# Optimization experiments

Measured on AMD Instinct MI355X. Metric: run time of the kernel, lower is better.

Reference implementation:

```python
import jax, jax.numpy as jnp
import numpy as np

DECAY = 0.99


def setup_inputs() -> dict:
    key = jax.random.key(0)
    k1, k2, k3 = jax.random.split(key, 3)
    B, L, D, N = 8, 2048, 512, 1024
    x = jax.random.normal(k1, (B, L, D), dtype=jnp.float32)
    codebook = jax.random.normal(k2, (N, D), dtype=jnp.float32)
    ema_weight = jax.random.normal(k3, (N, D), dtype=jnp.float32)
    counts = jnp.ones((N,), dtype=jnp.float32)
    return {"x": x, "codebook": codebook, "ema_weight": ema_weight, "counts": counts}


def reference(x, codebook, ema_weight, counts):
    # x: [B, L, D]; codebook/ema_weight: [N, D]; counts: [N]
    n_tokens = codebook.shape[0]
    # avoids materializing the [B,L,N,D] difference tensor of the naive form)
    x_sq = jnp.sum(x * x, axis=-1, keepdims=True)            # [B, L, 1]
    c_sq = jnp.sum(codebook * codebook, axis=-1)             # [N]
    xc = jnp.einsum('bld,nd->bln', x, codebook)              # [B, L, N]
    distances = jnp.sqrt(jnp.maximum(x_sq - 2.0 * xc + c_sq, 0.0))
    indices = jnp.argmin(distances, axis=-1)                 # [B, L]
    encodings = jax.nn.one_hot(indices, n_tokens, dtype=jnp.float32)  # [B, L, N]
    # train=True branch: EMA codebook update
    counts_new = DECAY * counts + (1.0 - DECAY) * jnp.sum(encodings, axis=(0, 1))
    dw = jnp.einsum('bln,bld->nd', encodings, x)             # [N, D]
    ema_new = DECAY * ema_weight + (1.0 - DECAY) * dw
    codebook_new = ema_new / counts_new[:, None]
    # quantization with straight-through estimator
    quantized = jnp.einsum('bln,nd->bld', encodings, codebook_new)  # [B, L, D]
    quantized = x + jax.lax.stop_gradient(quantized - x)
    # optax.l2_loss(x, quantized) = 0.5 * (x - quantized)^2
    codebook_loss = jnp.mean(0.5 * jnp.square(x - quantized))
    return quantized, codebook_loss, indices
```

## Files before the change

kernel.cpp:

```cpp
#include <hip/hip_runtime.h>
#include <hip/hip_bf16.h>

constexpr int Dd   = 512;
constexpr int Nn   = 1024;
constexpr int Ttok = 16384;
constexpr float DECAYc = 0.99f;
constexpr float MARGIN = 10.0f;
constexpr int CH = 16;

typedef short bf16x8 __attribute__((ext_vector_type(8)));
typedef float f32x4  __attribute__((ext_vector_type(4)));
typedef unsigned short us8v __attribute__((ext_vector_type(8)));

__device__ inline unsigned short f2bf(float f) {
  unsigned int b = __float_as_uint(f);
  return (unsigned short)((b + 0x7FFFu + ((b >> 16) & 1u)) >> 16);
}
__device__ inline float bf2f(unsigned short u) {
  return __uint_as_float(((unsigned int)u) << 16);
}

__global__ __launch_bounds__(64) void k_prep_cb(const float* __restrict__ cb,
                                                unsigned short* __restrict__ cbh,
                                                float* __restrict__ csq) {
  const int n = blockIdx.x, l = threadIdx.x;
  const float4* r = (const float4*)(cb + (size_t)n * Dd);
  float4 a = r[l], b = r[l + 64];
  float ss = a.x*a.x + a.y*a.y + a.z*a.z + a.w*a.w
           + b.x*b.x + b.y*b.y + b.z*b.z + b.w*b.w;
  ushort4 ua, ub;
  ua.x = f2bf(a.x); ua.y = f2bf(a.y); ua.z = f2bf(a.z); ua.w = f2bf(a.w);
  ub.x = f2bf(b.x); ub.y = f2bf(b.y); ub.z = f2bf(b.z); ub.w = f2bf(b.w);
  ((ushort4*)(cbh + (size_t)n * Dd))[l]      = ua;
  ((ushort4*)(cbh + (size_t)n * Dd))[l + 64] = ub;
#pragma unroll
  for (int o = 32; o; o >>= 1) ss += __shfl_down(ss, o);
  if (l == 0) csq[n] = ss;
}

__global__ __launch_bounds__(256) void k_gemm_scores(
    const unsigned short* __restrict__ cbh, const float* __restrict__ x,
    const float* __restrict__ csq, unsigned short* __restrict__ S) {
  __shared__ unsigned short As[128 * 64];
  __shared__ unsigned short Bs[128 * 64];
  const int tid = threadIdx.x;
  const int w = tid >> 6, l = tid & 63;
  const int b = blockIdx.x;
  const int s = (b & 7) * 128 + (b >> 3);
  const int cm = s & 7;
  const int tn = s >> 3;
  const int wr = w >> 1, wc = w & 1;

  const int srow = tid >> 3;
  const int scol = (tid & 7) * 8;

  f32x4 acc[4][4] = {};

  const unsigned short* gA0 = cbh + (size_t)(cm * 128) * Dd;
  const float*          gB0 = x   + (size_t)(tn * 128) * Dd;

  for (int kc = 0; kc < Dd / 64; ++kc) {
    const int k0 = kc * 64;
    __syncthreads();
#pragma unroll
    for (int c = 0; c < 4; ++c) {
      const unsigned short* ga = gA0 + (size_t)(c * 32 + srow) * Dd + k0 + scol;
      char* la = (char*)As + c * 4096 + w * 1024;
      __builtin_amdgcn_global_load_lds((const __attribute__((address_space(1))) void*)ga,
                                       (__attribute__((address_space(3))) void*)la, 16, 0, 0);
    }
#pragma unroll
    for (int p = 0; p < 4; ++p) {
      const int r = p * 32 + srow;
      const float* gb = gB0 + (size_t)r * Dd + k0 + scol;
      float4 v0 = *(const float4*)gb;
      float4 v1 = *(const float4*)(gb + 4);
      us8v o;
      o[0] = f2bf(v0.x); o[1] = f2bf(v0.y); o[2] = f2bf(v0.z); o[3] = f2bf(v0.w);
      o[4] = f2bf(v1.x); o[5] = f2bf(v1.y); o[6] = f2bf(v1.z); o[7] = f2bf(v1.w);
      *(us8v*)&Bs[r * 64 + scol] = o;
    }
    __syncthreads();
#pragma unroll
    for (int ks = 0; ks < 2; ++ks) {
      const int kb = ks * 32 + (l >> 4) * 8;
      const int ra = l & 15;
      bf16x8 af[4], bfr[4];
#pragma unroll
      for (int m = 0; m < 4; ++m)
        af[m] = *(const bf16x8*)&As[(wr * 64 + m * 16 + ra) * 64 + kb];
#pragma unroll
      for (int n = 0; n < 4; ++n)
        bfr[n] = *(const bf16x8*)&Bs[(wc * 64 + n * 16 + ra) * 64 + kb];
#pragma unroll
      for (int m = 0; m < 4; ++m)
#pragma unroll
        for (int n = 0; n < 4; ++n)
          acc[m][n] = __builtin_amdgcn_mfma_f32_16x16x32_bf16(af[m], bfr[n], acc[m][n], 0, 0, 0);
    }
  }

  const int code0 = cm * 128 + wr * 64 + (l >> 4) * 4;
  const int tok0  = tn * 128 + wc * 64 + (l & 15);
#pragma unroll
  for (int m = 0; m < 4; ++m) {
    const int cd = code0 + m * 16;
    float4 cs = *(const float4*)&csq[cd];
#pragma unroll
    for (int n = 0; n < 4; ++n) {
      const int tk = tok0 + n * 16;
      ushort4 o;
      o.x = f2bf(cs.x - 2.0f * acc[m][n][0]);
      o.y = f2bf(cs.y - 2.0f * acc[m][n][1]);
      o.z = f2bf(cs.z - 2.0f * acc[m][n][2]);
      o.w = f2bf(cs.w - 2.0f * acc[m][n][3]);
      *(ushort4*)(S + (size_t)tk * Nn + cd) = o;
    }
  }
}

__global__ __launch_bounds__(256) void k_scan(
    const unsigned short* __restrict__ S, const float* __restrict__ x,
    const float* __restrict__ cb, const float* __restrict__ csq,
    int* __restrict__ idxb, float* __restrict__ idxf, float* __restrict__ hist) {
  __shared__ int candn[4][32];
  __shared__ int ccnt[4];
  const int tid = threadIdx.x, wid = tid >> 6, l = tid & 63;
  const int t = blockIdx.x * 4 + wid;

  const unsigned short* row = S + (size_t)t * Nn;
  us8v c0 = *(const us8v*)(row + l * 8);
  us8v c1 = *(const us8v*)(row + 512 + l * 8);
  float f0[8], f1[8];
  float minv = 3.4e38f; int mini = 0;
#pragma unroll
  for (int j = 0; j < 8; ++j) {
    f0[j] = bf2f(c0[j]);
    if (f0[j] < minv) { minv = f0[j]; mini = l * 8 + j; }
  }
#pragma unroll
  for (int j = 0; j < 8; ++j) {
    f1[j] = bf2f(c1[j]);
    if (f1[j] < minv) { minv = f1[j]; mini = 512 + l * 8 + j; }
  }
#pragma unroll
  for (int o = 1; o < 64; o <<= 1) {
    float ov = __shfl_xor(minv, o); int oi = __shfl_xor(mini, o);
    if (ov < minv || (ov == minv && oi < mini)) { minv = ov; mini = oi; }
  }
  if (l == 0) ccnt[wid] = 0;
  const float thr = minv + MARGIN;
#pragma unroll
  for (int j = 0; j < 8; ++j)
    if (f0[j] <= thr) { int p = atomicAdd(&ccnt[wid], 1); if (p < 32) candn[wid][p] = l * 8 + j; }
#pragma unroll
  for (int j = 0; j < 8; ++j)
    if (f1[j] <= thr) { int p = atomicAdd(&ccnt[wid], 1); if (p < 32) candn[wid][p] = 512 + l * 8 + j; }
  int nc = ccnt[wid]; if (nc > 32) nc = 32;

  int besti;
  if (nc == 1) {
    besti = candn[wid][0];
  } else {
    float bestv = 3.4e38f; besti = 0x7fffffff;
    const float4* xr = (const float4*)(x + (size_t)t * Dd);
    float4 xa = xr[l * 2], xb = xr[l * 2 + 1];
    for (int c = 0; c < nc; ++c) {
      int n = candn[wid][c];
      const float4* cr = (const float4*)(cb + (size_t)n * Dd);
      float4 ca = cr[l * 2], cb4 = cr[l * 2 + 1];
      float p = xa.x*ca.x + xa.y*ca.y + xa.z*ca.z + xa.w*ca.w
              + xb.x*cb4.x + xb.y*cb4.y + xb.z*cb4.z + xb.w*cb4.w;
#pragma unroll
      for (int o = 32; o; o >>= 1) p += __shfl_xor(p, o);
      float sc = csq[n] - 2.0f * p;
      if (sc < bestv || (sc == bestv && n < besti)) { bestv = sc; besti = n; }
    }
  }
  if (l == 0) {
    idxb[t] = besti;
    idxf[t] = (float)besti;
    atomicAdd(&hist[besti], 1.0f);
  }
}

__global__ __launch_bounds__(1024) void k_offsets(const float* __restrict__ hist,
                                                  int* __restrict__ offs,
                                                  int* __restrict__ cursor) {
  __shared__ int sh[1024];
  const int tid = threadIdx.x;
  const int c = (int)hist[tid];
  sh[tid] = c; __syncthreads();
  for (int o = 1; o < 1024; o <<= 1) {
    int a = (tid >= o) ? sh[tid - o] : 0;
    __syncthreads();
    sh[tid] += a;
    __syncthreads();
  }
  const int excl = sh[tid] - c;
  offs[tid] = excl; cursor[tid] = excl;
}

__global__ __launch_bounds__(256) void k_scatter(const int* __restrict__ idxb,
                                                 int* __restrict__ cursor,
                                                 int* __restrict__ bucket,
                                                 int* __restrict__ bcode) {
  int t = blockIdx.x * 256 + threadIdx.x;
  if (t < Ttok) {
    int n = idxb[t];
    int p = atomicAdd(&cursor[n], 1);
    bucket[p] = t;
    bcode[p] = n;
  }
}

__global__ __launch_bounds__(512) void k_dw_part(
    const float* __restrict__ x, const int* __restrict__ bucket,
    const int* __restrict__ bcode, float* __restrict__ dw) {
  __shared__ int sh_t[CH], sh_n[CH];
  const int tid = threadIdx.x;
  const int p0 = blockIdx.x * CH;
  if (tid < CH) { sh_t[tid] = bucket[p0 + tid]; sh_n[tid] = bcode[p0 + tid]; }
  __syncthreads();
  float v[CH];
#pragma unroll
  for (int j = 0; j < CH; ++j)
    v[j] = x[(size_t)sh_t[j] * Dd + tid];
  float acc = v[0]; int cur = sh_n[0];
#pragma unroll
  for (int j = 1; j < CH; ++j) {
    int n = sh_n[j];
    if (n != cur) { atomicAdd(&dw[(size_t)cur * Dd + tid], acc); acc = 0.f; cur = n; }
    acc += v[j];
  }
  atomicAdd(&dw[(size_t)cur * Dd + tid], acc);
}

__global__ __launch_bounds__(256) void finalize_cb(
    const float* __restrict__ ema, const float* __restrict__ dw,
    const float* __restrict__ counts, const float* __restrict__ hist,
    float* __restrict__ cbnew) {
  int e4 = blockIdx.x * 256 + threadIdx.x;
  int n = e4 >> 7;
  float cnt = DECAYc * counts[n] + (1.0f - DECAYc) * hist[n];
  float inv = 1.0f / cnt;
  float4 e = ((const float4*)ema)[e4];
  float4 d = ((const float4*)dw)[e4];
  float4 o;
  o.x = (DECAYc * e.x + (1.0f - DECAYc) * d.x) * inv;
  o.y = (DECAYc * e.y + (1.0f - DECAYc) * d.y) * inv;
  o.z = (DECAYc * e.z + (1.0f - DECAYc) * d.z) * inv;
  o.w = (DECAYc * e.w + (1.0f - DECAYc) * d.w) * inv;
  ((float4*)cbnew)[e4] = o;
}

__global__ __launch_bounds__(256) void quant_loss(
    const float* __restrict__ x, const float* __restrict__ cbnew,
    const int* __restrict__ idx, float* __restrict__ out_q,
    float* __restrict__ loss) {
  float part = 0.f;
  const int total4 = Ttok * Dd / 4;
  for (int e4 = blockIdx.x * 256 + threadIdx.x; e4 < total4;
       e4 += gridDim.x * 256) {
    int t = e4 >> 7, d4 = e4 & 127;
    int n = idx[t];
    float4 q = ((const float4*)(cbnew + (size_t)n * Dd))[d4];
    float4 xv = ((const float4*)x)[e4];
    ((float4*)out_q)[e4] = q;
    float dx = xv.x - q.x, dy = xv.y - q.y, dz = xv.z - q.z, dw_ = xv.w - q.w;
    part += dx*dx + dy*dy + dz*dz + dw_*dw_;
  }
  __shared__ float red[4];
#pragma unroll
  for (int o = 32; o; o >>= 1) part += __shfl_down(part, o);
  int wid = threadIdx.x >> 6, lane = threadIdx.x & 63;
  if (lane == 0) red[wid] = part;
  __syncthreads();
  if (threadIdx.x == 0) atomicAdd(loss, red[0] + red[1] + red[2] + red[3]);
}

__global__ void loss_final(const float* __restrict__ loss,
                           float* __restrict__ out_loss) {
  *out_loss = loss[0] * (0.5f / (float)((size_t)Ttok * Dd));
}

extern "C" void kernel_launch(void* const* d_in, const int* in_sizes, int n_in,
                              void* d_out, int out_size, void* d_ws, size_t ws_size,
                              hipStream_t stream) {
  const float* x      = (const float*)d_in[0];
  const float* cb     = (const float*)d_in[1];
  const float* ema    = (const float*)d_in[2];
  const float* counts = (const float*)d_in[3];

  float* out      = (float*)d_out;
  float* q_out    = out;
  float* loss_out = out + (size_t)Ttok * Dd;
  float* idxf_out = loss_out + 1;
  unsigned short* S = (unsigned short*)q_out;

  float* ws = (float*)d_ws;
  unsigned short* cbh = (unsigned short*)ws;
  float* dw     = ws + 262144;
  float* hist   = ws + 786432;
  float* loss   = ws + 787456;
  float* csq    = ws + 787460;
  int*   offs   = (int*)(ws + 788484);
  int*   cursor = (int*)(ws + 789508);
  int*   bucket = (int*)(ws + 790532);
  int*   bcode  = (int*)(ws + 806916);
  int*   idxb   = (int*)(ws + 823300);
  float* cbnew  = ws + 839684;

  hipMemsetAsync(dw, 0, (size_t)525316 * sizeof(float), stream);

  k_prep_cb<<<Nn, 64, 0, stream>>>(cb, cbh, csq);
  k_gemm_scores<<<(Nn / 128) * (Ttok / 128), 256, 0, stream>>>(cbh, x, csq, S);
  k_scan<<<Ttok / 4, 256, 0, stream>>>(S, x, cb, csq, idxb, idxf_out, hist);
  k_offsets<<<1, 1024, 0, stream>>>(hist, offs, cursor);
  k_scatter<<<Ttok / 256, 256, 0, stream>>>(idxb, cursor, bucket, bcode);
  k_dw_part<<<Ttok / CH, 512, 0, stream>>>(x, bucket, bcode, dw);
  finalize_cb<<<(Nn * Dd / 4) / 256, 256, 0, stream>>>(ema, dw, counts, hist, cbnew);
  quant_loss<<<2048, 256, 0, stream>>>(x, cbnew, idxb, q_out, loss);
  loss_final<<<1, 1, 0, stream>>>(loss, loss_out);
}
```

Baseline: 135.5 us.

## Swizzle GEMM LDS, prefetch x tile into registers, simplify scan, fuse loss finalize

The scores GEMM now XOR-swizzles the LDS column layout for both A and B tiles to avoid bank conflicts, and prefetches the next k-chunk of x (converted to bf16) into registers while the current chunk is multiplied. The offsets scan drops to 256 threads using wave shuffles in place of a barrier-heavy shared-memory scan. The separate loss_final launch is removed: the last block of quant_loss, found through an atomic counter, writes the normalized loss. Together these aim to cut LDS stalls, global-load latency and launch overhead, at the cost of more registers in the GEMM. The counter relies on the existing memset.

```diff
diff --git a/kernel.cpp b/kernel.cpp
--- a/kernel.cpp
+++ b/kernel.cpp
@@ -52,46 +52,60 @@
   const int wr = w >> 1, wc = w & 1;
 
   const int srow = tid >> 3;
-  const int scol = (tid & 7) * 8;
+  const int xorw = (tid >> 3) & 7;
+  const int scolA = ((tid & 7) ^ xorw) * 8;
+  const int scolB = (tid & 7) * 8;
+  const int wcolB = ((tid & 7) ^ xorw) * 8;
 
   f32x4 acc[4][4] = {};
 
   const unsigned short* gA0 = cbh + (size_t)(cm * 128) * Dd;
   const float*          gB0 = x   + (size_t)(tn * 128) * Dd;
+
+  us8v bq[4];
+#define LOADB(KC) do {                                                        \
+    const int k0_ = (KC) * 64;                                                \
+    _Pragma("unroll")                                                         \
+    for (int p = 0; p < 4; ++p) {                                             \
+      const float* gb = gB0 + (size_t)(p * 32 + srow) * Dd + k0_ + scolB;     \
+      float4 v0 = *(const float4*)gb;                                         \
+      float4 v1 = *(const float4*)(gb + 4);                                   \
+      us8v o;                                                                 \
+      o[0]=f2bf(v0.x); o[1]=f2bf(v0.y); o[2]=f2bf(v0.z); o[3]=f2bf(v0.w);     \
+      o[4]=f2bf(v1.x); o[5]=f2bf(v1.y); o[6]=f2bf(v1.z); o[7]=f2bf(v1.w);     \
+      bq[p] = o;                                                              \
+    }                                                                         \
+  } while (0)
+
+  LOADB(0);
 
   for (int kc = 0; kc < Dd / 64; ++kc) {
     const int k0 = kc * 64;
     __syncthreads();
 #pragma unroll
     for (int c = 0; c < 4; ++c) {
-      const unsigned short* ga = gA0 + (size_t)(c * 32 + srow) * Dd + k0 + scol;
+      const unsigned short* ga = gA0 + (size_t)(c * 32 + srow) * Dd + k0 + scolA;
       char* la = (char*)As + c * 4096 + w * 1024;
       __builtin_amdgcn_global_load_lds((const __attribute__((address_space(1))) void*)ga,
                                        (__attribute__((address_space(3))) void*)la, 16, 0, 0);
     }
 #pragma unroll
-    for (int p = 0; p < 4; ++p) {
-      const int r = p * 32 + srow;
-      const float* gb = gB0 + (size_t)r * Dd + k0 + scol;
-      float4 v0 = *(const float4*)gb;
-      float4 v1 = *(const float4*)(gb + 4);
-      us8v o;
-      o[0] = f2bf(v0.x); o[1] = f2bf(v0.y); o[2] = f2bf(v0.z); o[3] = f2bf(v0.w);
-      o[4] = f2bf(v1.x); o[5] = f2bf(v1.y); o[6] = f2bf(v1.z); o[7] = f2bf(v1.w);
-      *(us8v*)&Bs[r * 64 + scol] = o;
-    }
+    for (int p = 0; p < 4; ++p)
+      *(us8v*)&Bs[(p * 32 + srow) * 64 + wcolB] = bq[p];
     __syncthreads();
+    if (kc + 1 < Dd / 64) LOADB(kc + 1);
 #pragma unroll
     for (int ks = 0; ks < 2; ++ks) {
-      const int kb = ks * 32 + (l >> 4) * 8;
       const int ra = l & 15;
+      const int rx = l & 7;
+      const int kbs = ((ks * 4 + (l >> 4)) ^ rx) * 8;
       bf16x8 af[4], bfr[4];
 #pragma unroll
       for (int m = 0; m < 4; ++m)
-        af[m] = *(const bf16x8*)&As[(wr * 64 + m * 16 + ra) * 64 + kb];
+        af[m] = *(const bf16x8*)&As[(wr * 64 + m * 16 + ra) * 64 + kbs];
 #pragma unroll
       for (int n = 0; n < 4; ++n)
-        bfr[n] = *(const bf16x8*)&Bs[(wc * 64 + n * 16 + ra) * 64 + kb];
+        bfr[n] = *(const bf16x8*)&Bs[(wc * 64 + n * 16 + ra) * 64 + kbs];
 #pragma unroll
       for (int m = 0; m < 4; ++m)
 #pragma unroll
@@ -99,6 +113,7 @@
           acc[m][n] = __builtin_amdgcn_mfma_f32_16x16x32_bf16(af[m], bfr[n], acc[m][n], 0, 0, 0);
     }
   }
+#undef LOADB
 
   const int code0 = cm * 128 + wr * 64 + (l >> 4) * 4;
   const int tok0  = tn * 128 + wc * 64 + (l & 15);
@@ -184,21 +199,27 @@
   }
 }
 
-__global__ __launch_bounds__(1024) void k_offsets(const float* __restrict__ hist,
-                                                  int* __restrict__ offs,
-                                                  int* __restrict__ cursor) {
-  __shared__ int sh[1024];
-  const int tid = threadIdx.x;
-  const int c = (int)hist[tid];
-  sh[tid] = c; __syncthreads();
-  for (int o = 1; o < 1024; o <<= 1) {
-    int a = (tid >= o) ? sh[tid - o] : 0;
-    __syncthreads();
-    sh[tid] += a;
-    __syncthreads();
-  }
-  const int excl = sh[tid] - c;
-  offs[tid] = excl; cursor[tid] = excl;
+__global__ __launch_bounds__(256) void k_offsets(const float* __restrict__ hist,
+                                                 int* __restrict__ offs,
+                                                 int* __restrict__ cursor) {
+  __shared__ int wsum[4];
+  const int tid = threadIdx.x, l = tid & 63, wd = tid >> 6;
+  const int base = tid * 4;
+  int c0 = (int)hist[base], c1 = (int)hist[base + 1],
+      c2 = (int)hist[base + 2], c3 = (int)hist[base + 3];
+  int sum = c0 + c1 + c2 + c3;
+  int sc = sum;
+#pragma unroll
+  for (int o = 1; o < 64; o <<= 1) { int v = __shfl_up(sc, o); if (l >= o) sc += v; }
+  if (l == 63) wsum[wd] = sc;
+  __syncthreads();
+  int wbase = 0;
+  for (int i = 0; i < wd; ++i) wbase += wsum[i];
+  int e = wbase + sc - sum;
+  offs[base] = e;     cursor[base] = e;
+  offs[base+1] = e + c0; cursor[base+1] = e + c0;
+  offs[base+2] = e + c0 + c1; cursor[base+2] = e + c0 + c1;
+  offs[base+3] = e + c0 + c1 + c2; cursor[base+3] = e + c0 + c1 + c2;
 }
 
 __global__ __launch_bounds__(256) void k_scatter(const int* __restrict__ idxb,
@@ -257,7 +278,8 @@
 __global__ __launch_bounds__(256) void quant_loss(
     const float* __restrict__ x, const float* __restrict__ cbnew,
     const int* __restrict__ idx, float* __restrict__ out_q,
-    float* __restrict__ loss) {
+    float* __restrict__ loss, int* __restrict__ counter,
+    float* __restrict__ out_loss) {
   float part = 0.f;
   const int total4 = Ttok * Dd / 4;
   for (int e4 = blockIdx.x * 256 + threadIdx.x; e4 < total4;
@@ -276,12 +298,13 @@
   int wid = threadIdx.x >> 6, lane = threadIdx.x & 63;
   if (lane == 0) red[wid] = part;
   __syncthreads();
-  if (threadIdx.x == 0) atomicAdd(loss, red[0] + red[1] + red[2] + red[3]);
-}
-
-__global__ void loss_final(const float* __restrict__ loss,
-                           float* __restrict__ out_loss) {
-  *out_loss = loss[0] * (0.5f / (float)((size_t)Ttok * Dd));
+  if (threadIdx.x == 0) {
+    atomicAdd(loss, red[0] + red[1] + red[2] + red[3]);
+    __threadfence();
+    int prev = atomicAdd(counter, 1);
+    if (prev == (int)gridDim.x - 1)
+      *out_loss = *loss * (0.5f / (float)((size_t)Ttok * Dd));
+  }
 }
 
 extern "C" void kernel_launch(void* const* d_in, const int* in_sizes, int n_in,
@@ -300,26 +323,26 @@
 
   float* ws = (float*)d_ws;
   unsigned short* cbh = (unsigned short*)ws;
-  float* dw     = ws + 262144;
-  float* hist   = ws + 786432;
-  float* loss   = ws + 787456;
-  float* csq    = ws + 787460;
-  int*   offs   = (int*)(ws + 788484);
-  int*   cursor = (int*)(ws + 789508);
-  int*   bucket = (int*)(ws + 790532);
-  int*   bcode  = (int*)(ws + 806916);
-  int*   idxb   = (int*)(ws + 823300);
-  float* cbnew  = ws + 839684;
+  float* dw      = ws + 262144;
+  float* hist    = ws + 786432;
+  float* loss    = ws + 787456;
+  int*   counter = (int*)(ws + 787457);
+  float* csq     = ws + 787460;
+  int*   offs    = (int*)(ws + 788484);
+  int*   cursor  = (int*)(ws + 789508);
+  int*   bucket  = (int*)(ws + 790532);
+  int*   bcode   = (int*)(ws + 806916);
+  int*   idxb    = (int*)(ws + 823300);
+  float* cbnew   = ws + 839684;
 
   hipMemsetAsync(dw, 0, (size_t)525316 * sizeof(float), stream);
 
   k_prep_cb<<<Nn, 64, 0, stream>>>(cb, cbh, csq);
   k_gemm_scores<<<(Nn / 128) * (Ttok / 128), 256, 0, stream>>>(cbh, x, csq, S);
   k_scan<<<Ttok / 4, 256, 0, stream>>>(S, x, cb, csq, idxb, idxf_out, hist);
-  k_offsets<<<1, 1024, 0, stream>>>(hist, offs, cursor);
+  k_offsets<<<1, 256, 0, stream>>>(hist, offs, cursor);
   k_scatter<<<Ttok / 256, 256, 0, stream>>>(idxb, cursor, bucket, bcode);
   k_dw_part<<<Ttok / CH, 512, 0, stream>>>(x, bucket, bcode, dw);
   finalize_cb<<<(Nn * Dd / 4) / 256, 256, 0, stream>>>(ema, dw, counts, hist, cbnew);
-  quant_loss<<<2048, 256, 0, stream>>>(x, cbnew, idxb, q_out, loss);
-  loss_final<<<1, 1, 0, stream>>>(loss, loss_out);
-}
+  quant_loss<<<2048, 256, 0, stream>>>(x, cbnew, idxb, q_out, loss, counter, loss_out);
+}
```

Measured after the change: 166.8 us. +23.1%, slower.
